# Optimization experiments

Measured on AMD Instinct MI355X. Metric: run time of the kernel, lower is better.

Reference implementation:

```python
import jax, jax.numpy as jnp
import numpy as np

N_DIM = 32
N_HEADS = 4
HEAD_SIZE = N_DIM // N_HEADS  # 8


def setup_inputs() -> dict:
    key = jax.random.key(0)
    ks = jax.random.split(key, 9)
    B, T = 16, 2048
    s = 1.0 / np.sqrt(N_DIM)
    inp = {
        "x": jax.random.normal(ks[0], (B, T, N_DIM), dtype=jnp.float32),
        "Wq": jax.random.uniform(ks[1], (N_DIM, N_DIM), jnp.float32, -s, s),
        "bq": jax.random.uniform(ks[2], (N_DIM,), jnp.float32, -s, s),
        "Wk": jax.random.uniform(ks[3], (N_DIM, N_DIM), jnp.float32, -s, s),
        "bk": jax.random.uniform(ks[4], (N_DIM,), jnp.float32, -s, s),
        "Wv": jax.random.uniform(ks[5], (N_DIM, N_DIM), jnp.float32, -s, s),
        "bv": jax.random.uniform(ks[6], (N_DIM,), jnp.float32, -s, s),
        "Wp": jax.random.uniform(ks[7], (N_DIM, N_DIM), jnp.float32, -s, s),
        "bp": jax.random.uniform(ks[8], (N_DIM,), jnp.float32, -s, s),
    }
    return inp


def reference(x, Wq, bq, Wk, bk, Wv, bv, Wp, bp):
    b, t, c = x.shape
    # nn.Linear: y = x @ W^T + b
    def heads(W, bias):
        y = jnp.einsum("btc,dc->btd", x, W) + bias
        return y.reshape(b, t, N_HEADS, HEAD_SIZE).transpose(0, 2, 1, 3)  # [b,h,t,d]

    q = heads(Wq, bq)
    k = heads(Wk, bk)
    v = heads(Wv, bv)

    scores = jnp.einsum("bhqd,bhkd->bhqk", q, k) / np.sqrt(HEAD_SIZE)  # [b,h,t,t]
    causal = jnp.tril(jnp.ones((t, t), dtype=bool))
    scores = jnp.where(causal[None, None], scores, -jnp.inf)
    weights = jax.nn.softmax(scores, axis=-1)
    # dropout layers are identity in eval mode
    z = jnp.einsum("bhqk,bhkd->bhqd", weights, v)
    z = z.transpose(0, 2, 1, 3).reshape(b, t, N_DIM)
    z = jnp.einsum("btc,dc->btd", z, Wp) + bp
    return z
```

## Files before the change

kernel.cpp:

```cpp
#include <hip/hip_runtime.h>
#include <math.h>

#define BB 16
#define TT 2048
#define CC 32
#define HH 4
#define DD 8

#define KBS2 1040
#define VRS2 136
#define VBS2 (9 * VRS2)
#define ZP 33

typedef __fp16 h2  __attribute__((ext_vector_type(2)));
typedef __fp16 h8  __attribute__((ext_vector_type(8)));
typedef float  fx16 __attribute__((ext_vector_type(16)));
typedef int    i4v __attribute__((ext_vector_type(4)));
typedef int    i2v __attribute__((ext_vector_type(2)));

__device__ __forceinline__ h2 pkh(float a, float b) {
#if __has_builtin(__builtin_amdgcn_cvt_pkrtz)
    return __builtin_amdgcn_cvt_pkrtz(a, b);
#else
    h2 r; r.x = (__fp16)a; r.y = (__fp16)b; return r;
#endif
}

__device__ __forceinline__ float fexp2(float x) {
#if __has_builtin(__builtin_amdgcn_exp2f)
    return __builtin_amdgcn_exp2f(x);
#else
    return exp2f(x);
#endif
}

__device__ __forceinline__ int h2bits(h2 v) { return __builtin_bit_cast(int, v); }

__device__ __forceinline__ h8 pk8(float4 a, float4 b) {
    i4v f;
    f.x = h2bits(pkh(a.x, a.y)); f.y = h2bits(pkh(a.z, a.w));
    f.z = h2bits(pkh(b.x, b.y)); f.w = h2bits(pkh(b.z, b.w));
    return __builtin_bit_cast(h8, f);
}

__device__ __forceinline__ void makeP(const fx16& S, bool last, int thr, int hi, h8* P) {
    float pe[16];
    #pragma unroll
    for (int r = 0; r < 16; r++) {
        const int ko = (r & 3) + 8 * (r >> 2);
        float sv = S[r];
        if (last) sv = (ko <= thr) ? sv : -INFINITY;
        pe[r] = fexp2(sv);
    }
    int Hh[8];
    #pragma unroll
    for (int i = 0; i < 8; i++) Hh[i] = h2bits(pkh(pe[2*i], pe[2*i+1]));
#if __has_builtin(__builtin_amdgcn_permlane32_swap)
    #pragma unroll
    for (int s = 0; s < 2; s++) {
        const int b0 = 4 * s;
        auto ra = __builtin_amdgcn_permlane32_swap(Hh[b0+0], Hh[b0+2], false, false);
        auto rb = __builtin_amdgcn_permlane32_swap(Hh[b0+1], Hh[b0+3], false, false);
        i2v pa = __builtin_bit_cast(i2v, ra);
        i2v pb = __builtin_bit_cast(i2v, rb);
        i4v f;
        f.x = pa.x; f.y = pb.x; f.z = pa.y; f.w = pb.y;
        P[s] = __builtin_bit_cast(h8, f);
    }
#else
    #pragma unroll
    for (int s = 0; s < 2; s++) {
        const int b0 = 4 * s;
        int own0 = hi ? Hh[b0+2] : Hh[b0+0];
        int own1 = hi ? Hh[b0+3] : Hh[b0+1];
        int snd0 = hi ? Hh[b0+0] : Hh[b0+2];
        int snd1 = hi ? Hh[b0+1] : Hh[b0+3];
        int rcv0 = __shfl_xor(snd0, 32);
        int rcv1 = __shfl_xor(snd1, 32);
        i4v f;
        f.x = hi ? rcv0 : own0;
        f.y = hi ? rcv1 : own1;
        f.z = hi ? own0 : rcv0;
        f.w = hi ? own1 : rcv1;
        P[s] = __builtin_bit_cast(h8, f);
    }
#endif
}

__global__ __launch_bounds__(192, 3) void qkv_kernel(
    const float* __restrict__ x,
    const float* __restrict__ Wq, const float* __restrict__ bq,
    const float* __restrict__ Wk, const float* __restrict__ bk,
    const float* __restrict__ Wv, const float* __restrict__ bv,
    __fp16* __restrict__ Qo, __fp16* __restrict__ Ko, __fp16* __restrict__ Vo)
{
    const int tid  = threadIdx.x;
    const int m    = tid >> 6;
    const int lane = tid & 63;
    const int qc   = lane & 31;
    const int hi   = lane >> 5;

    const int row = blockIdx.x * 32 + qc;
    const int b   = row >> 11, t = row & 2047;

    const float* W    = (m == 0) ? Wq : (m == 1) ? Wk : Wv;
    const float* bias = (m == 0) ? bq : (m == 1) ? bk : bv;

    const float* xr = x + (size_t)row * CC + 8 * hi;
    h8 B0 = pk8(*(const float4*)(xr),      *(const float4*)(xr + 4));
    h8 B1 = pk8(*(const float4*)(xr + 16), *(const float4*)(xr + 20));

    const float* wr = W + (size_t)qc * CC + 8 * hi;
    h8 A0 = pk8(*(const float4*)(wr),      *(const float4*)(wr + 4));
    h8 A1 = pk8(*(const float4*)(wr + 16), *(const float4*)(wr + 20));

    fx16 zc;
    #pragma unroll
    for (int i = 0; i < 16; i++) zc[i] = 0.0f;
    fx16 D = __builtin_amdgcn_mfma_f32_32x32x16_f16(A0, B0, zc, 0, 0, 0);
    D = __builtin_amdgcn_mfma_f32_32x32x16_f16(A1, B1, D, 0, 0, 0);

    float o[16];
    {
        float4 bb0 = *(const float4*)(bias + 0  + 4 * hi);
        float4 bb1 = *(const float4*)(bias + 8  + 4 * hi);
        float4 bb2 = *(const float4*)(bias + 16 + 4 * hi);
        float4 bb3 = *(const float4*)(bias + 24 + 4 * hi);
        o[0] = D[0] + bb0.x; o[1] = D[1] + bb0.y; o[2]  = D[2]  + bb0.z; o[3]  = D[3]  + bb0.w;
        o[4] = D[4] + bb1.x; o[5] = D[5] + bb1.y; o[6]  = D[6]  + bb1.z; o[7]  = D[7]  + bb1.w;
        o[8] = D[8] + bb2.x; o[9] = D[9] + bb2.y; o[10] = D[10] + bb2.z; o[11] = D[11] + bb2.w;
        o[12] = D[12] + bb3.x; o[13] = D[13] + bb3.y; o[14] = D[14] + bb3.z; o[15] = D[15] + bb3.w;
    }
    if (m == 0) {
        const float qs = 0.3535533905932738f * 1.4426950408889634f;
        #pragma unroll
        for (int r = 0; r < 16; r++) o[r] *= qs;
    }

    if (m == 2) {
        #pragma unroll
        for (int r = 0; r < 16; r++) {
            const int h = r >> 2, d = (r & 3) + 4 * hi;
            Vo[(((size_t)(b * HH + h)) * 9 + d) * TT + t] = (__fp16)o[r];
        }
        const int hA = hi ? 2 : 0, hB = hi ? 3 : 1;
        Vo[(((size_t)(b * HH + hA)) * 9 + 8) * TT + t] = (__fp16)1.0f;
        Vo[(((size_t)(b * HH + hB)) * 9 + 8) * TT + t] = (__fp16)1.0f;
    } else {
        int I0[4], I1[4];
        #pragma unroll
        for (int g = 0; g < 4; g++) {
            I0[g] = h2bits(pkh(o[4*g + 0], o[4*g + 1]));
            I1[g] = h2bits(pkh(o[4*g + 2], o[4*g + 3]));
        }
        i4v fr0, fr1, fr2, fr3;
#if __has_builtin(__builtin_amdgcn_permlane32_swap)
    #define MAKE_FRAG(g, out) { \
        auto ra = __builtin_amdgcn_permlane32_swap(I0[g], I1[g], false, false); \
        auto rb = __builtin_amdgcn_permlane32_swap(I1[g], I0[g], false, false); \
        i2v p1 = __builtin_bit_cast(i2v, ra); \
        i2v p2 = __builtin_bit_cast(i2v, rb); \
        i4v f; \
        f.x = hi ? p2.x : p1.x; \
        f.y = hi ? p1.x : p2.x; \
        f.z = hi ? p2.y : p1.y; \
        f.w = hi ? p1.y : p2.y; \
        out = f; }
#else
    #define MAKE_FRAG(g, out) { \
        int s0 = __shfl_xor(I0[g], 32); \
        int s1 = __shfl_xor(I1[g], 32); \
        i4v f; \
        f.x = hi ? s0 : I0[g]; \
        f.y = hi ? s1 : I1[g]; \
        f.z = hi ? I0[g] : s0; \
        f.w = hi ? I1[g] : s1; \
        out = f; }
#endif
        MAKE_FRAG(0, fr0); MAKE_FRAG(1, fr1); MAKE_FRAG(2, fr2); MAKE_FRAG(3, fr3);
    #undef MAKE_FRAG
        i4v fA = hi ? fr2 : fr0;
        i4v fB = hi ? fr3 : fr1;
        const int gA = hi ? 2 : 0, gB = hi ? 3 : 1;
        __fp16* O = (m == 0) ? Qo : Ko;
        *(i4v*)(O + ((size_t)(b * HH + gA) * TT + t) * DD) = fA;
        *(i4v*)(O + ((size_t)(b * HH + gB) * TT + t) * DD) = fB;
    }
}

__global__ __launch_bounds__(512, 4) void attn_kernel(
    const __fp16* __restrict__ Qg, const __fp16* __restrict__ Kg,
    const __fp16* __restrict__ Vg,
    const float* __restrict__ Wp, const float* __restrict__ bp,
    float* __restrict__ out)
{
    __shared__ __align__(16) __fp16 KsS[8 * KBS2];
    __shared__ __align__(16) __fp16 VtS[8 * VBS2];
    __shared__ float zA[64 * ZP];
    __shared__ float zB[64 * ZP];
    __shared__ float lA[64 * 4];
    __shared__ float lB[64 * 4];

    const int tid  = threadIdx.x;
    const int b    = blockIdx.x & 15;
    const int ip   = blockIdx.x >> 4;
    const int w    = tid >> 6;
    const int h    = w & 3;
    const int hsel = w >> 2;
    const int lane = tid & 63;
    const int qc   = lane & 31;
    const int hi   = lane >> 5;

    const int bh  = b * HH + h;
    const int qb1 = 32 * ip;
    const int qb2 = 32 * (63 - ip);
    const int stile = (ip < 15) ? (31 - ip) : 16;
    const int ks = hsel ? stile * 32 : 0;
    const int ke = hsel ? (64 - ip) * 32 : stile * 32;

    h8 qf1, qf2;
    {
        h8 qz;
        #pragma unroll
        for (int i = 0; i < 8; i++) qz[i] = (__fp16)0.0f;
        h8 qa = *(const h8*)(Qg + ((size_t)bh * TT + qb1 + qc) * DD);
        h8 qb = *(const h8*)(Qg + ((size_t)bh * TT + qb2 + qc) * DD);
        qf1 = hi ? qz : qa;
        qf2 = hi ? qz : qb;
    }

    fx16 O1, O2, zc;
    #pragma unroll
    for (int i = 0; i < 16; i++) { O1[i] = 0.0f; O2[i] = 0.0f; zc[i] = 0.0f; }

    const int vrow = (qc < 9) ? qc : 8;
    const int thr  = qc - 4 * hi;

    const __fp16* kgl = Kg + (size_t)bh * TT * DD;
    const __fp16* vgl = Vg + (size_t)bh * 9 * TT;
    __fp16* kld = KsS + w * KBS2;
    __fp16* vld = VtS + w * VBS2;
    const __fp16* kb = kld + qc * DD;
    const __fp16* vb = vld + vrow * VRS2 + 8 * hi;

    const int nst = (ke - ks + 127) >> 7;

    i4v kpre[2], vpre[3];
    {
        #pragma unroll
        for (int r = 0; r < 2; r++) {
            int row = ks + lane + 64 * r; if (row > TT - 1) row = TT - 1;
            kpre[r] = *(const i4v*)(kgl + (size_t)row * DD);
        }
        #pragma unroll
        for (int r = 0; r < 3; r++) {
            int i = lane + 64 * r; if (i > 143) i = 143;
            int col = ks + (i & 15) * 8; if (col > TT - 8) col = TT - 8;
            vpre[r] = *(const i4v*)(vgl + (i >> 4) * TT + col);
        }
    }

    for (int sti = 0; sti < nst; sti++) {
        const int st = ks + sti * 128;
        {
            i4v* kd = (i4v*)kld;
            #pragma unroll
            for (int r = 0; r < 2; r++) kd[lane + 64 * r] = kpre[r];
            #pragma unroll
            for (int r = 0; r < 3; r++) {
                const int i = lane + 64 * r;
                if (i < 144) *(i4v*)(vld + (i >> 4) * VRS2 + (i & 15) * 8) = vpre[r];
            }
        }
        if (sti + 1 < nst) {
            const int st2 = st + 128;
            #pragma unroll
            for (int r = 0; r < 2; r++) {
                int row = st2 + lane + 64 * r; if (row > TT - 1) row = TT - 1;
                kpre[r] = *(const i4v*)(kgl + (size_t)row * DD);
            }
            #pragma unroll
            for (int r = 0; r < 3; r++) {
                int i = lane + 64 * r; if (i > 143) i = 143;
                int col = st2 + (i & 15) * 8; if (col > TT - 8) col = TT - 8;
                vpre[r] = *(const i4v*)(vgl + (i >> 4) * TT + col);
            }
        }

        const int kend = min(st + 128, ke);
        for (int kt = st; kt < kend; kt += 32) {
            const bool a1 = (kt <= qb1);
            h8 kf = *(const h8*)(kb + (kt - st) * DD);

            h8 P1[2], P2[2];
            if (a1) {
                fx16 S = __builtin_amdgcn_mfma_f32_32x32x16_f16(kf, qf1, zc, 0, 0, 0);
                makeP(S, kt == qb1, thr, hi, P1);
            }
            {
                fx16 S = __builtin_amdgcn_mfma_f32_32x32x16_f16(kf, qf2, zc, 0, 0, 0);
                makeP(S, kt == qb2, thr, hi, P2);
            }
            #pragma unroll
            for (int s = 0; s < 2; s++) {
                h8 vf = *(const h8*)(vb + (kt - st) + 16 * s);
                if (a1) O1 = __builtin_amdgcn_mfma_f32_32x32x16_f16(vf, P1[s], O1, 0, 0, 0);
                O2 = __builtin_amdgcn_mfma_f32_32x32x16_f16(vf, P2[s], O2, 0, 0, 0);
            }
        }
    }

    {
        float* zW = hsel ? zB : zA;
        float* lW = hsel ? lB : lA;
        float* z1 = &zW[qc * ZP + h * DD + 4 * hi];
        float* z2 = &zW[(32 + qc) * ZP + h * DD + 4 * hi];
        z1[0] = O1[0]; z1[1] = O1[1]; z1[2] = O1[2]; z1[3] = O1[3];
        z2[0] = O2[0]; z2[1] = O2[1]; z2[2] = O2[2]; z2[3] = O2[3];
        lW[qc * 4 + h] = O1[4];
        lW[(32 + qc) * 4 + h] = O2[4];
    }
    __syncthreads();

    {
        const int seg = tid >> 6;
        const int r = tid & 63;
        float linv[4];
        #pragma unroll
        for (int hh = 0; hh < 4; hh++)
            linv[hh] = 1.0f / (lA[r * 4 + hh] + lB[r * 4 + hh]);
        float zr[CC];
        #pragma unroll
        for (int c = 0; c < CC; c++)
            zr[c] = (zA[r * ZP + c] + zB[r * ZP + c]) * linv[c >> 3];
        float o[4];
        #pragma unroll
        for (int d = 0; d < 4; d++) {
            const int dd = seg * 4 + d;
            float acc = bp[dd];
            #pragma unroll
            for (int c = 0; c < CC; c++) acc += zr[c] * Wp[dd * CC + c];
            o[d] = acc;
        }
        const int qglob = (r < 32) ? (ip * 32 + r) : ((63 - ip) * 32 + (r - 32));
        float* dst = out + ((size_t)b * TT + qglob) * CC + seg * 4;
        *(float4*)dst = make_float4(o[0], o[1], o[2], o[3]);
    }
}

extern "C" void kernel_launch(void* const* d_in, const int* in_sizes, int n_in,
                              void* d_out, int out_size, void* d_ws, size_t ws_size,
                              hipStream_t stream) {
    const float* x  = (const float*)d_in[0];
    const float* Wq = (const float*)d_in[1];
    const float* bq = (const float*)d_in[2];
    const float* Wk = (const float*)d_in[3];
    const float* bk = (const float*)d_in[4];
    const float* Wv = (const float*)d_in[5];
    const float* bv = (const float*)d_in[6];
    const float* Wp = (const float*)d_in[7];
    const float* bp = (const float*)d_in[8];
    float* out = (float*)d_out;

    const size_t NE = (size_t)BB * HH * TT * DD;
    __fp16* Qh = (__fp16*)d_ws;
    __fp16* Kh = Qh + NE;
    __fp16* Vt = Kh + NE;

    qkv_kernel<<<dim3(BB * TT / 32), 192, 0, stream>>>(x, Wq, bq, Wk, bk, Wv, bv, Qh, Kh, Vt);
    attn_kernel<<<dim3(BB * 32), 512, 0, stream>>>(Qh, Kh, Vt, Wp, bp, out);
}
```

Measured before the change: 105.4 us.

## Rebalance causal attention work split between wave halves per query pair

Replaces the fused dual-query-tile sweep with separate sweeps. The first half of the waves handles the late query tile over keys [0,1056). The second half handles the rest of that tile and then the whole early query tile. This drops the per-iteration a1 predicate and the duplicated score MFMA per key tile, and keeps the work per wave half near constant. The cost is that K/V tiles are loaded twice for keys the two query tiles share, zB/lB must be zeroed up front, and the second half runs two serial sweeps.

```diff
diff --git a/kernel.cpp b/kernel.cpp
--- a/kernel.cpp
+++ b/kernel.cpp
@@ -188,6 +188,69 @@
     }
 }
 
+__device__ __forceinline__ void sweep(
+    const __fp16* __restrict__ kgl, const __fp16* __restrict__ vgl,
+    __fp16* kld, __fp16* vld, const __fp16* kb, const __fp16* vb,
+    int ks, int ke, int qb, h8 qf, int thr, int hi, int lane,
+    fx16& O, const fx16& zc)
+{
+    if (ks >= ke) return;
+    const int nst = (ke - ks + 127) >> 7;
+    i4v kpre[2], vpre[3];
+    {
+        #pragma unroll
+        for (int r = 0; r < 2; r++) {
+            int row = ks + lane + 64 * r; if (row > TT - 1) row = TT - 1;
+            kpre[r] = *(const i4v*)(kgl + (size_t)row * DD);
+        }
+        #pragma unroll
+        for (int r = 0; r < 3; r++) {
+            int i = lane + 64 * r; if (i > 143) i = 143;
+            int col = ks + (i & 15) * 8; if (col > TT - 8) col = TT - 8;
+            vpre[r] = *(const i4v*)(vgl + (i >> 4) * TT + col);
+        }
+    }
+    for (int sti = 0; sti < nst; sti++) {
+        const int st = ks + sti * 128;
+        {
+            i4v* kd = (i4v*)kld;
+            #pragma unroll
+            for (int r = 0; r < 2; r++) kd[lane + 64 * r] = kpre[r];
+            #pragma unroll
+            for (int r = 0; r < 3; r++) {
+                const int i = lane + 64 * r;
+                if (i < 144) *(i4v*)(vld + (i >> 4) * VRS2 + (i & 15) * 8) = vpre[r];
+            }
+        }
+        if (sti + 1 < nst) {
+            const int st2 = st + 128;
+            #pragma unroll
+            for (int r = 0; r < 2; r++) {
+                int row = st2 + lane + 64 * r; if (row > TT - 1) row = TT - 1;
+                kpre[r] = *(const i4v*)(kgl + (size_t)row * DD);
+            }
+            #pragma unroll
+            for (int r = 0; r < 3; r++) {
+                int i = lane + 64 * r; if (i > 143) i = 143;
+                int col = st2 + (i & 15) * 8; if (col > TT - 8) col = TT - 8;
+                vpre[r] = *(const i4v*)(vgl + (i >> 4) * TT + col);
+            }
+        }
+        const int kend = min(st + 128, ke);
+        for (int kt = st; kt < kend; kt += 32) {
+            h8 kf = *(const h8*)(kb + (kt - st) * DD);
+            fx16 S = __builtin_amdgcn_mfma_f32_32x32x16_f16(kf, qf, zc, 0, 0, 0);
+            h8 P[2];
+            makeP(S, kt == qb, thr, hi, P);
+            #pragma unroll
+            for (int s = 0; s < 2; s++) {
+                h8 vf = *(const h8*)(vb + (kt - st) + 16 * s);
+                O = __builtin_amdgcn_mfma_f32_32x32x16_f16(vf, P[s], O, 0, 0, 0);
+            }
+        }
+    }
+}
+
 __global__ __launch_bounds__(512, 4) void attn_kernel(
     const __fp16* __restrict__ Qg, const __fp16* __restrict__ Kg,
     const __fp16* __restrict__ Vg,
@@ -206,7 +269,7 @@
     const int ip   = blockIdx.x >> 4;
     const int w    = tid >> 6;
     const int h    = w & 3;
-    const int hsel = w >> 2;
+    const int half = w >> 2;
     const int lane = tid & 63;
     const int qc   = lane & 31;
     const int hi   = lane >> 5;
@@ -214,9 +277,13 @@
     const int bh  = b * HH + h;
     const int qb1 = 32 * ip;
     const int qb2 = 32 * (63 - ip);
-    const int stile = (ip < 15) ? (31 - ip) : 16;
-    const int ks = hsel ? stile * 32 : 0;
-    const int ke = hsel ? (64 - ip) * 32 : stile * 32;
+
+    for (int i = tid; i < 32 * ZP; i += 512) zB[i] = 0.0f;
+    if (tid < 128) lB[tid] = 0.0f;
+    if (ip == 31) {
+        for (int i = tid; i < 32 * ZP; i += 512) zB[32 * ZP + i] = 0.0f;
+        if (tid < 128) lB[128 + tid] = 0.0f;
+    }
 
     h8 qf1, qf2;
     {
@@ -229,9 +296,9 @@
         qf2 = hi ? qz : qb;
     }
 
-    fx16 O1, O2, zc;
-    #pragma unroll
-    for (int i = 0; i < 16; i++) { O1[i] = 0.0f; O2[i] = 0.0f; zc[i] = 0.0f; }
+    fx16 O, zc;
+    #pragma unroll
+    for (int i = 0; i < 16; i++) { O[i] = 0.0f; zc[i] = 0.0f; }
 
     const int vrow = (qc < 9) ? qc : 8;
     const int thr  = qc - 4 * hi;
@@ -243,82 +310,26 @@
     const __fp16* kb = kld + qc * DD;
     const __fp16* vb = vld + vrow * VRS2 + 8 * hi;
 
-    const int nst = (ke - ks + 127) >> 7;
-
-    i4v kpre[2], vpre[3];
-    {
-        #pragma unroll
-        for (int r = 0; r < 2; r++) {
-            int row = ks + lane + 64 * r; if (row > TT - 1) row = TT - 1;
-            kpre[r] = *(const i4v*)(kgl + (size_t)row * DD);
-        }
-        #pragma unroll
-        for (int r = 0; r < 3; r++) {
-            int i = lane + 64 * r; if (i > 143) i = 143;
-            int col = ks + (i & 15) * 8; if (col > TT - 8) col = TT - 8;
-            vpre[r] = *(const i4v*)(vgl + (i >> 4) * TT + col);
-        }
-    }
-
-    for (int sti = 0; sti < nst; sti++) {
-        const int st = ks + sti * 128;
-        {
-            i4v* kd = (i4v*)kld;
-            #pragma unroll
-            for (int r = 0; r < 2; r++) kd[lane + 64 * r] = kpre[r];
-            #pragma unroll
-            for (int r = 0; r < 3; r++) {
-                const int i = lane + 64 * r;
-                if (i < 144) *(i4v*)(vld + (i >> 4) * VRS2 + (i & 15) * 8) = vpre[r];
-            }
-        }
-        if (sti + 1 < nst) {
-            const int st2 = st + 128;
-            #pragma unroll
-            for (int r = 0; r < 2; r++) {
-                int row = st2 + lane + 64 * r; if (row > TT - 1) row = TT - 1;
-                kpre[r] = *(const i4v*)(kgl + (size_t)row * DD);
-            }
-            #pragma unroll
-            for (int r = 0; r < 3; r++) {
-                int i = lane + 64 * r; if (i > 143) i = 143;
-                int col = st2 + (i & 15) * 8; if (col > TT - 8) col = TT - 8;
-                vpre[r] = *(const i4v*)(vgl + (i >> 4) * TT + col);
-            }
-        }
-
-        const int kend = min(st + 128, ke);
-        for (int kt = st; kt < kend; kt += 32) {
-            const bool a1 = (kt <= qb1);
-            h8 kf = *(const h8*)(kb + (kt - st) * DD);
-
-            h8 P1[2], P2[2];
-            if (a1) {
-                fx16 S = __builtin_amdgcn_mfma_f32_32x32x16_f16(kf, qf1, zc, 0, 0, 0);
-                makeP(S, kt == qb1, thr, hi, P1);
-            }
-            {
-                fx16 S = __builtin_amdgcn_mfma_f32_32x32x16_f16(kf, qf2, zc, 0, 0, 0);
-                makeP(S, kt == qb2, thr, hi, P2);
-            }
-            #pragma unroll
-            for (int s = 0; s < 2; s++) {
-                h8 vf = *(const h8*)(vb + (kt - st) + 16 * s);
-                if (a1) O1 = __builtin_amdgcn_mfma_f32_32x32x16_f16(vf, P1[s], O1, 0, 0, 0);
-                O2 = __builtin_amdgcn_mfma_f32_32x32x16_f16(vf, P2[s], O2, 0, 0, 0);
-            }
-        }
-    }
-
-    {
-        float* zW = hsel ? zB : zA;
-        float* lW = hsel ? lB : lA;
-        float* z1 = &zW[qc * ZP + h * DD + 4 * hi];
-        float* z2 = &zW[(32 + qc) * ZP + h * DD + 4 * hi];
-        z1[0] = O1[0]; z1[1] = O1[1]; z1[2] = O1[2]; z1[3] = O1[3];
-        z2[0] = O2[0]; z2[1] = O2[1]; z2[2] = O2[2]; z2[3] = O2[3];
-        lW[qc * 4 + h] = O1[4];
-        lW[(32 + qc) * 4 + h] = O2[4];
+    if (half == 0) {
+        sweep(kgl, vgl, kld, vld, kb, vb, 0, 1056, qb2, qf2, thr, hi, lane, O, zc);
+        float* z = &zA[(32 + qc) * ZP + h * DD + 4 * hi];
+        z[0] = O[0]; z[1] = O[1]; z[2] = O[2]; z[3] = O[3];
+        lA[(32 + qc) * 4 + h] = O[4];
+    } else {
+        sweep(kgl, vgl, kld, vld, kb, vb, 1056, (64 - ip) * 32, qb2, qf2,
+              thr, hi, lane, O, zc);
+        if (ip < 31) {
+            float* z = &zB[(32 + qc) * ZP + h * DD + 4 * hi];
+            z[0] = O[0]; z[1] = O[1]; z[2] = O[2]; z[3] = O[3];
+            lB[(32 + qc) * 4 + h] = O[4];
+            #pragma unroll
+            for (int i = 0; i < 16; i++) O[i] = 0.0f;
+        }
+        sweep(kgl, vgl, kld, vld, kb, vb, 0, (ip + 1) * 32, qb1, qf1,
+              thr, hi, lane, O, zc);
+        float* z = &zA[qc * ZP + h * DD + 4 * hi];
+        z[0] = O[0]; z[1] = O[1]; z[2] = O[2]; z[3] = O[3];
+        lA[qc * 4 + h] = O[4];
     }
     __syncthreads();
 
```

New measurement: 107.5 us. No clear change (+2.0%).
